# Kernel tuning notes

Hardware: AMD Instinct MI355X
Metric: run time of the kernel (lower is better)

The kernel has to match this reference:

```python
import jax, jax.numpy as jnp
import numpy as np

N_CLUSTERS = 1024
EMBED_DIM = 256
BETA = 0.25
EPS = 1e-05


def setup_inputs() -> dict:
    key = jax.random.key(0)
    k1, k2 = jax.random.split(key)
    z = jax.random.normal(k1, (16, 64, 64, EMBED_DIM), dtype=jnp.float32)
    # nn.init.uniform_(codebook, -1/K, 1/K)
    bound = 1.0 / N_CLUSTERS
    codebook = jax.random.uniform(k2, (N_CLUSTERS, EMBED_DIM), dtype=jnp.float32,
                                  minval=-bound, maxval=bound)
    return {"z": z, "codebook": codebook}


def reference(z, codebook):
    K = codebook.shape[0]
    # squared distances: ||z||^2 + ||e||^2 - 2 z.e  -> [B,V,P,K]
    z2 = jnp.sum(z * z, axis=-1, keepdims=True)          # [B,V,P,1]
    e2 = jnp.sum(codebook * codebook, axis=-1)           # [K]
    ze = jnp.einsum('bvpd,kd->bvpk', z, codebook)        # [B,V,P,K]
    dist = z2 + e2[None, None, None, :] - 2.0 * ze
    indices = jnp.argmin(dist, axis=-1)                  # [B,V,P] int
    z_q = codebook[indices]                              # gather [B,V,P,D]
    z_q_st = z + jax.lax.stop_gradient(z_q - z)          # straight-through

    codebook_loss = jnp.mean((z_q - jax.lax.stop_gradient(z)) ** 2)
    commitment_loss = jnp.mean((z - jax.lax.stop_gradient(z_q)) ** 2)
    cluster_loss = codebook_loss + BETA * commitment_loss

    # perplexity stats (no grad)
    counts = jnp.zeros((K,), dtype=jnp.float32).at[indices.ravel()].add(1.0)
    probs = counts / (counts.sum() + EPS)
    perplexity = jnp.exp(-jnp.sum(probs * jnp.log(probs + EPS)))

    return z_q_st, commitment_loss, codebook_loss, cluster_loss, perplexity, indices
```

## Files before the change

kernel.cpp:

```cpp
#include <hip/hip_runtime.h>
#include <cfloat>
#include <math.h>

#define P_TOT 65536
#define DIM   256
#define KTOT  1024
#define BETA_ 0.25f
#define EPS_  1e-5f
#define MARGIN_ 1.5e-4f

#define OUT_LOSS_OFF ((size_t)P_TOT * DIM)
#define OUT_IDX_OFF  (OUT_LOSS_OFF + 4)

typedef __attribute__((ext_vector_type(8))) short s16x8;
typedef __attribute__((ext_vector_type(4))) float f32x4;

__device__ __forceinline__ unsigned short f2bf(float x) {
    unsigned u = __float_as_uint(x);
    u += 0x7FFFu + ((u >> 16) & 1u);
    return (unsigned short)(u >> 16);
}
__device__ __forceinline__ float bf2f(unsigned short h) {
    return __uint_as_float(((unsigned)h) << 16);
}
__device__ __forceinline__ void gl16(const void* g, void* l) {
    __builtin_amdgcn_global_load_lds(
        (const __attribute__((address_space(1))) unsigned int*)g,
        (__attribute__((address_space(3))) unsigned int*)l, 16, 0, 0);
}

__global__ __launch_bounds__(64) void vq_prep(const float* __restrict__ cb,
                                              float* __restrict__ e2,
                                              unsigned short* __restrict__ cbh,
                                              unsigned short* __restrict__ cbl,
                                              unsigned int* __restrict__ hist,
                                              float* __restrict__ loss_sum,
                                              unsigned int* __restrict__ flag_cnt) {
    const int k = blockIdx.x;
    const int lane = threadIdx.x;
    float4 v = *(const float4*)(cb + (size_t)k * DIM + lane * 4);
    float s = v.x * v.x + v.y * v.y + v.z * v.z + v.w * v.w;
    #pragma unroll
    for (int off = 32; off > 0; off >>= 1) s += __shfl_down(s, off, 64);
    if (lane == 0) e2[k] = s;

    unsigned short h0 = f2bf(v.x), h1 = f2bf(v.y), h2 = f2bf(v.z), h3 = f2bf(v.w);
    unsigned short l0 = f2bf(v.x - bf2f(h0)), l1 = f2bf(v.y - bf2f(h1));
    unsigned short l2 = f2bf(v.z - bf2f(h2)), l3 = f2bf(v.w - bf2f(h3));
    uint2 hp, lp;
    hp.x = (unsigned)h0 | ((unsigned)h1 << 16); hp.y = (unsigned)h2 | ((unsigned)h3 << 16);
    lp.x = (unsigned)l0 | ((unsigned)l1 << 16); lp.y = (unsigned)l2 | ((unsigned)l3 << 16);
    *(uint2*)(cbh + (size_t)k * DIM + lane * 4) = hp;
    *(uint2*)(cbl + (size_t)k * DIM + lane * 4) = lp;

    const int gid = k * 64 + lane;
    if (gid < KTOT) hist[gid] = 0u;
    if (gid == KTOT) { *loss_sum = 0.0f; *flag_cnt = 0u; }
}

__global__ __launch_bounds__(256) void vq_zsplit(const float* __restrict__ z,
                                                 float* __restrict__ z2,
                                                 float* __restrict__ out) {
    const int lane = threadIdx.x & 63;
    const int wave = threadIdx.x >> 6;
    const int p = blockIdx.x * 4 + wave;
    float4 v = *(const float4*)(z + (size_t)p * DIM + lane * 4);
    float s = v.x * v.x + v.y * v.y + v.z * v.z + v.w * v.w;
    #pragma unroll
    for (int off = 32; off > 0; off >>= 1) s += __shfl_down(s, off, 64);
    if (lane == 0) z2[p] = s;

    unsigned short h0 = f2bf(v.x), h1 = f2bf(v.y), h2 = f2bf(v.z), h3 = f2bf(v.w);
    unsigned short l0 = f2bf(v.x - bf2f(h0)), l1 = f2bf(v.y - bf2f(h1));
    unsigned short l2 = f2bf(v.z - bf2f(h2)), l3 = f2bf(v.w - bf2f(h3));
    uint2 hp, lp;
    hp.x = (unsigned)h0 | ((unsigned)h1 << 16); hp.y = (unsigned)h2 | ((unsigned)h3 << 16);
    lp.x = (unsigned)l0 | ((unsigned)l1 << 16); lp.y = (unsigned)l2 | ((unsigned)l3 << 16);
    char* rowb = (char*)out + (size_t)p * 1024;
    *(uint2*)(rowb + lane * 8) = hp;
    *(uint2*)(rowb + 512 + lane * 8) = lp;
}

#define BM 128
#define BN 128

__global__ __launch_bounds__(256, 2) void vq_argmin(
    const float* __restrict__ z, const float* __restrict__ cb,
    const unsigned short* __restrict__ cbh, const unsigned short* __restrict__ cbl,
    const float* __restrict__ z2, const float* __restrict__ e2,
    unsigned int* __restrict__ hist, float* __restrict__ loss_sum,
    unsigned int* __restrict__ flag_cnt, unsigned int* __restrict__ flag_list,
    float* __restrict__ out)
{
    __shared__ __align__(16) char sm[65536];
    __shared__ int kwin[BM];
    __shared__ unsigned char flgs[BM];
    __shared__ float wred[4];

    const int tid = threadIdx.x;
    const int lane = tid & 63;
    const int wid = tid >> 6;
    const int wm = wid >> 1, wn = wid & 1;
    const int col = lane & 15;
    const int lg  = lane >> 4;
    const int swz = lane & 7;
    const int row0 = blockIdx.x * BM;

    const char* zsB  = (const char*)out;
    const char* cbhB = (const char*)cbh;
    const char* cblB = (const char*)cbl;

    float b1[16], b2[16]; int i1[16];
    float z2r[16];
    #pragma unroll
    for (int q = 0; q < 16; ++q) {
        b1[q] = FLT_MAX; b2[q] = FLT_MAX; i1[q] = 0;
        z2r[q] = z2[row0 + wm * 64 + (q >> 2) * 16 + lg * 4 + (q & 3)];
    }

    int aRow[4], bRow[4];
    #pragma unroll
    for (int f = 0; f < 4; ++f) {
        aRow[f] = (wm * 64 + f * 16 + col) * 128;
        bRow[f] = (wn * 64 + f * 16 + col) * 128;
    }
    const int bc0 = ((0 + lg) ^ swz) << 4;
    const int bc1 = ((4 + lg) ^ swz) << 4;

    const int sr  = lane >> 3;
    const int scb = lane & 7;

    #pragma unroll 1
    for (int nc = 0; nc < KTOT / BN; ++nc) {
        const int n0 = nc * BN;
        f32x4 acc[4][4];
        #pragma unroll
        for (int fm = 0; fm < 4; ++fm)
            #pragma unroll
            for (int fn = 0; fn < 4; ++fn)
                acc[fm][fn] = (f32x4){0.0f, 0.0f, 0.0f, 0.0f};

        #pragma unroll 1
        for (int kc = 0; kc < 4; ++kc) {
            __syncthreads();
            #pragma unroll
            for (int i = 0; i < 4; ++i) {
                const int rloc = wid * 32 + i * 8 + sr;
                const int cb16 = ((scb ^ (rloc & 7)) << 4);
                const size_t aoff = ((size_t)(row0 + rloc) << 10) + (kc << 7);
                const size_t boff = ((size_t)(n0 + rloc) << 9) + (kc << 7);
                char* lb = sm + (wid * 32 + i * 8) * 128;
                gl16(zsB + aoff + cb16,        lb);
                gl16(zsB + aoff + 512 + cb16,  lb + 16384);
                gl16(cbhB + boff + cb16,       lb + 32768);
                gl16(cblB + boff + cb16,       lb + 49152);
            }
            __syncthreads();
            #pragma unroll
            for (int ks = 0; ks < 2; ++ks) {
                const int bc = ks ? bc1 : bc0;
                s16x8 ah[4], al[4], bh[4], bl[4];
                #pragma unroll
                for (int f = 0; f < 4; ++f) {
                    ah[f] = *(const s16x8*)(sm + aRow[f] + bc);
                    al[f] = *(const s16x8*)(sm + 16384 + aRow[f] + bc);
                    bh[f] = *(const s16x8*)(sm + 32768 + bRow[f] + bc);
                    bl[f] = *(const s16x8*)(sm + 49152 + bRow[f] + bc);
                }
                #pragma unroll
                for (int fm = 0; fm < 4; ++fm)
                    #pragma unroll
                    for (int fn = 0; fn < 4; ++fn) {
                        acc[fm][fn] = __builtin_amdgcn_mfma_f32_16x16x32_bf16(
                            ah[fm], bh[fn], acc[fm][fn], 0, 0, 0);
                        acc[fm][fn] = __builtin_amdgcn_mfma_f32_16x16x32_bf16(
                            ah[fm], bl[fn], acc[fm][fn], 0, 0, 0);
                        acc[fm][fn] = __builtin_amdgcn_mfma_f32_16x16x32_bf16(
                            al[fm], bh[fn], acc[fm][fn], 0, 0, 0);
                    }
            }
        }
        float e2v[4];
        #pragma unroll
        for (int fn = 0; fn < 4; ++fn) e2v[fn] = e2[n0 + wn * 64 + fn * 16 + col];
        #pragma unroll
        for (int fm = 0; fm < 4; ++fm)
            #pragma unroll
            for (int fn = 0; fn < 4; ++fn)
                #pragma unroll
                for (int r4 = 0; r4 < 4; ++r4) {
                    const int q = fm * 4 + r4;
                    const float dist = (z2r[q] + e2v[fn]) - 2.0f * acc[fm][fn][r4];
                    const int idx = n0 + wn * 64 + fn * 16 + col;
                    if (dist < b1[q]) { b2[q] = b1[q]; b1[q] = dist; i1[q] = idx; }
                    else if (dist < b2[q]) { b2[q] = dist; }
                }
    }

    __syncthreads();
    float* Rb1 = (float*)sm;
    float* Rb2 = (float*)(sm + 16896);
    int*   Ri1 = (int*)(sm + 33792);
    const int slot = col + 16 * wn;
    #pragma unroll
    for (int q = 0; q < 16; ++q) {
        const int px = wm * 64 + (q >> 2) * 16 + lg * 4 + (q & 3);
        Rb1[px * 33 + slot] = b1[q];
        Rb2[px * 33 + slot] = b2[q];
        Ri1[px * 33 + slot] = i1[q];
    }
    __syncthreads();
    if (tid < BM) {
        float x1 = Rb1[tid * 33], x2 = Rb2[tid * 33]; int xi = Ri1[tid * 33];
        for (int s = 1; s < 32; ++s) {
            const float c1 = Rb1[tid * 33 + s], c2 = Rb2[tid * 33 + s];
            const int ci = Ri1[tid * 33 + s];
            const float nb2 = fminf(fmaxf(x1, c1), fminf(x2, c2));
            if (c1 < x1 || (c1 == x1 && ci < xi)) { x1 = c1; xi = ci; }
            x2 = nb2;
        }
        kwin[tid] = xi;
        const bool fl = (x2 - x1) <= MARGIN_;
        flgs[tid] = fl ? 1 : 0;
        if (fl) {
            const unsigned pos = atomicAdd(flag_cnt, 1u);
            flag_list[pos] = (unsigned)(row0 + tid);
        } else {
            out[OUT_IDX_OFF + row0 + tid] = (float)xi;
            atomicAdd(&hist[xi], 1u);
        }
    }
    __syncthreads();

    float lacc = 0.0f;
    #pragma unroll 4
    for (int i = 0; i < 32; ++i) {
        const int flat4 = tid + i * 256;
        const int row = flat4 >> 6;
        if (!flgs[row]) {
            const int dj = (flat4 & 63) * 4;
            const size_t zoff = (size_t)(row0 + row) * DIM + dj;
            float4 zv = *(const float4*)(z + zoff);
            float4 ev = *(const float4*)(cb + (size_t)kwin[row] * DIM + dj);
            float dx = ev.x - zv.x, dy = ev.y - zv.y, dz = ev.z - zv.z, dw = ev.w - zv.w;
            float4 o;
            o.x = zv.x + dx; o.y = zv.y + dy; o.z = zv.z + dz; o.w = zv.w + dw;
            *(float4*)(out + zoff) = o;
            lacc += dx * dx + dy * dy + dz * dz + dw * dw;
        }
    }
    #pragma unroll
    for (int off = 32; off > 0; off >>= 1) lacc += __shfl_down(lacc, off, 64);
    if (lane == 0) wred[wid] = lacc;
    __syncthreads();
    if (tid == 0) atomicAdd(loss_sum, wred[0] + wred[1] + wred[2] + wred[3]);
}

__global__ __launch_bounds__(256) void vq_fix(
    const float* __restrict__ z, const float* __restrict__ cb,
    const float* __restrict__ z2, const float* __restrict__ e2,
    const unsigned int* __restrict__ flag_cnt, const unsigned int* __restrict__ flag_list,
    unsigned int* __restrict__ hist, float* __restrict__ loss_sum,
    float* __restrict__ out)
{
    __shared__ float zrow[4][DIM];
    __shared__ float zz2[4];
    __shared__ int pxid[4];
    __shared__ float rb[4][256];
    __shared__ int   ri[4][256];
    __shared__ int   kw4[4];

    const int tid = threadIdx.x;
    const int total = (int)*flag_cnt;

    for (int base = blockIdx.x * 4; base < total; base += gridDim.x * 4) {
        const int npx = min(4, total - base);
        __syncthreads();
        if (tid < 4) {
            const int p = (int)flag_list[base + (tid < npx ? tid : 0)];
            pxid[tid] = p; zz2[tid] = z2[p];
        }
        __syncthreads();
        {
            const int q = tid >> 6, d = (tid & 63) * 4;
            float4 v = *(const float4*)(z + (size_t)pxid[q] * DIM + d);
            *(float4*)&zrow[q][d] = v;
        }
        __syncthreads();

        const int k0 = tid * 4;
        float acc[4][4];
        #pragma unroll
        for (int q = 0; q < 4; ++q)
            #pragma unroll
            for (int j = 0; j < 4; ++j) acc[q][j] = 0.0f;

        for (int d4 = 0; d4 < 64; ++d4) {
            float4 cv[4];
            #pragma unroll
            for (int j = 0; j < 4; ++j)
                cv[j] = *(const float4*)(cb + (size_t)(k0 + j) * DIM + d4 * 4);
            #pragma unroll
            for (int q = 0; q < 4; ++q) {
                float4 zv = *(const float4*)&zrow[q][d4 * 4];
                #pragma unroll
                for (int j = 0; j < 4; ++j) {
                    acc[q][j] = fmaf(zv.x, cv[j].x, acc[q][j]);
                    acc[q][j] = fmaf(zv.y, cv[j].y, acc[q][j]);
                    acc[q][j] = fmaf(zv.z, cv[j].z, acc[q][j]);
                    acc[q][j] = fmaf(zv.w, cv[j].w, acc[q][j]);
                }
            }
        }
        #pragma unroll
        for (int q = 0; q < 4; ++q) {
            float bd = FLT_MAX; int bi = 0;
            #pragma unroll
            for (int j = 0; j < 4; ++j) {
                const int k = k0 + j;
                const float dist = (zz2[q] + e2[k]) - 2.0f * acc[q][j];
                if (dist < bd) { bd = dist; bi = k; }
            }
            rb[q][tid] = bd; ri[q][tid] = bi;
        }
        __syncthreads();
        {
            const int q = tid >> 6, lane = tid & 63;
            float bd = rb[q][lane]; int bi = ri[q][lane];
            #pragma unroll
            for (int s = 1; s < 4; ++s) {
                const float d2 = rb[q][lane + s * 64]; const int i2 = ri[q][lane + s * 64];
                if (d2 < bd || (d2 == bd && i2 < bi)) { bd = d2; bi = i2; }
            }
            #pragma unroll
            for (int off = 32; off > 0; off >>= 1) {
                const float d2 = __shfl_down(bd, off, 64);
                const int i2 = __shfl_down(bi, off, 64);
                if (d2 < bd || (d2 == bd && i2 < bi)) { bd = d2; bi = i2; }
            }
            if (lane == 0) kw4[q] = bi;
        }
        __syncthreads();
        {
            const int q = tid >> 6, lane = tid & 63;
            if (q < npx) {
                const int p = pxid[q];
                const int kw = kw4[q];
                const int d = lane * 4;
                float4 zv = *(const float4*)&zrow[q][d];
                float4 ev = *(const float4*)(cb + (size_t)kw * DIM + d);
                float dx = ev.x - zv.x, dy = ev.y - zv.y, dz = ev.z - zv.z, dw = ev.w - zv.w;
                float4 o;
                o.x = zv.x + dx; o.y = zv.y + dy; o.z = zv.z + dz; o.w = zv.w + dw;
                *(float4*)(out + (size_t)p * DIM + d) = o;
                float lacc = dx * dx + dy * dy + dz * dz + dw * dw;
                #pragma unroll
                for (int off = 32; off > 0; off >>= 1) lacc += __shfl_down(lacc, off, 64);
                if (lane == 0) {
                    atomicAdd(loss_sum, lacc);
                    out[OUT_IDX_OFF + p] = (float)kw;
                    atomicAdd(&hist[kw], 1u);
                }
            }
        }
    }
}

__global__ __launch_bounds__(1024) void vq_finalize(
    const unsigned int* __restrict__ hist, const float* __restrict__ loss_sum,
    float* __restrict__ out)
{
    __shared__ float sred[16];
    __shared__ float totalsh;
    const int tid = threadIdx.x;
    const float c = (float)hist[tid];

    float t = c;
    #pragma unroll
    for (int off = 32; off > 0; off >>= 1) t += __shfl_down(t, off, 64);
    if ((tid & 63) == 0) sred[tid >> 6] = t;
    __syncthreads();
    if (tid == 0) {
        float s = 0.0f;
        for (int i = 0; i < 16; ++i) s += sred[i];
        totalsh = s;
    }
    __syncthreads();
    const float total = totalsh;
    const float prob = c / (total + EPS_);
    float term = prob * logf(prob + EPS_);
    __syncthreads();
    #pragma unroll
    for (int off = 32; off > 0; off >>= 1) term += __shfl_down(term, off, 64);
    if ((tid & 63) == 0) sred[tid >> 6] = term;
    __syncthreads();
    if (tid == 0) {
        float s = 0.0f;
        for (int i = 0; i < 16; ++i) s += sred[i];
        const float perp = expf(-s);
        const float S = *loss_sum;
        const float mean = S / (float)(P_TOT * DIM);
        out[OUT_LOSS_OFF + 0] = mean;
        out[OUT_LOSS_OFF + 1] = mean;
        out[OUT_LOSS_OFF + 2] = mean + BETA_ * mean;
        out[OUT_LOSS_OFF + 3] = perp;
    }
}

extern "C" void kernel_launch(void* const* d_in, const int* in_sizes, int n_in,
                              void* d_out, int out_size, void* d_ws, size_t ws_size,
                              hipStream_t stream) {
    const float* z  = (const float*)d_in[0];
    const float* cb = (const float*)d_in[1];
    float* out = (float*)d_out;

    float* z2 = (float*)d_ws;
    float* e2 = z2 + P_TOT;
    unsigned int* hist = (unsigned int*)(e2 + KTOT);
    float* loss_sum = (float*)(hist + KTOT);
    unsigned int* flag_cnt = (unsigned int*)(loss_sum + 1);
    unsigned int* flag_list = flag_cnt + 1;
    unsigned short* cbh = (unsigned short*)(((uintptr_t)(flag_list + P_TOT) + 15) & ~(uintptr_t)15);
    unsigned short* cbl = cbh + (size_t)KTOT * DIM;

    vq_prep<<<KTOT, 64, 0, stream>>>(cb, e2, cbh, cbl, hist, loss_sum, flag_cnt);
    vq_zsplit<<<P_TOT / 4, 256, 0, stream>>>(z, z2, out);
    vq_argmin<<<P_TOT / BM, 256, 0, stream>>>(z, cb, cbh, cbl, z2, e2,
                                              hist, loss_sum, flag_cnt, flag_list, out);
    vq_fix<<<1024, 256, 0, stream>>>(z, cb, z2, e2, flag_cnt, flag_list,
                                     hist, loss_sum, out);
    vq_finalize<<<1, 1024, 0, stream>>>(hist, loss_sum, out);
}
```

Measured before the change: 381.8 us.

## Double-buffer LDS staging in argmin GEMM and merge prep kernels

```diff
diff --git a/kernel.cpp b/kernel.cpp
--- a/kernel.cpp
+++ b/kernel.cpp
@@ -29,56 +29,57 @@
         (__attribute__((address_space(3))) unsigned int*)l, 16, 0, 0);
 }
 
-__global__ __launch_bounds__(64) void vq_prep(const float* __restrict__ cb,
-                                              float* __restrict__ e2,
-                                              unsigned short* __restrict__ cbh,
-                                              unsigned short* __restrict__ cbl,
-                                              unsigned int* __restrict__ hist,
-                                              float* __restrict__ loss_sum,
-                                              unsigned int* __restrict__ flag_cnt) {
-    const int k = blockIdx.x;
-    const int lane = threadIdx.x;
-    float4 v = *(const float4*)(cb + (size_t)k * DIM + lane * 4);
-    float s = v.x * v.x + v.y * v.y + v.z * v.z + v.w * v.w;
-    #pragma unroll
-    for (int off = 32; off > 0; off >>= 1) s += __shfl_down(s, off, 64);
-    if (lane == 0) e2[k] = s;
-
-    unsigned short h0 = f2bf(v.x), h1 = f2bf(v.y), h2 = f2bf(v.z), h3 = f2bf(v.w);
-    unsigned short l0 = f2bf(v.x - bf2f(h0)), l1 = f2bf(v.y - bf2f(h1));
-    unsigned short l2 = f2bf(v.z - bf2f(h2)), l3 = f2bf(v.w - bf2f(h3));
-    uint2 hp, lp;
-    hp.x = (unsigned)h0 | ((unsigned)h1 << 16); hp.y = (unsigned)h2 | ((unsigned)h3 << 16);
-    lp.x = (unsigned)l0 | ((unsigned)l1 << 16); lp.y = (unsigned)l2 | ((unsigned)l3 << 16);
-    *(uint2*)(cbh + (size_t)k * DIM + lane * 4) = hp;
-    *(uint2*)(cbl + (size_t)k * DIM + lane * 4) = lp;
-
-    const int gid = k * 64 + lane;
-    if (gid < KTOT) hist[gid] = 0u;
-    if (gid == KTOT) { *loss_sum = 0.0f; *flag_cnt = 0u; }
-}
-
-__global__ __launch_bounds__(256) void vq_zsplit(const float* __restrict__ z,
-                                                 float* __restrict__ z2,
-                                                 float* __restrict__ out) {
-    const int lane = threadIdx.x & 63;
-    const int wave = threadIdx.x >> 6;
-    const int p = blockIdx.x * 4 + wave;
-    float4 v = *(const float4*)(z + (size_t)p * DIM + lane * 4);
-    float s = v.x * v.x + v.y * v.y + v.z * v.z + v.w * v.w;
-    #pragma unroll
-    for (int off = 32; off > 0; off >>= 1) s += __shfl_down(s, off, 64);
-    if (lane == 0) z2[p] = s;
-
-    unsigned short h0 = f2bf(v.x), h1 = f2bf(v.y), h2 = f2bf(v.z), h3 = f2bf(v.w);
-    unsigned short l0 = f2bf(v.x - bf2f(h0)), l1 = f2bf(v.y - bf2f(h1));
-    unsigned short l2 = f2bf(v.z - bf2f(h2)), l3 = f2bf(v.w - bf2f(h3));
-    uint2 hp, lp;
-    hp.x = (unsigned)h0 | ((unsigned)h1 << 16); hp.y = (unsigned)h2 | ((unsigned)h3 << 16);
-    lp.x = (unsigned)l0 | ((unsigned)l1 << 16); lp.y = (unsigned)l2 | ((unsigned)l3 << 16);
-    char* rowb = (char*)out + (size_t)p * 1024;
-    *(uint2*)(rowb + lane * 8) = hp;
-    *(uint2*)(rowb + 512 + lane * 8) = lp;
+__global__ __launch_bounds__(256) void vq_pre(
+    const float* __restrict__ z, const float* __restrict__ cb,
+    float* __restrict__ z2, float* __restrict__ e2,
+    char* __restrict__ cbi, unsigned int* __restrict__ hist,
+    float* __restrict__ loss_sum, unsigned int* __restrict__ flag_cnt,
+    float* __restrict__ out)
+{
+    const int tid = threadIdx.x;
+    const int lane = tid & 63;
+    const int wave = tid >> 6;
+    const int bid = blockIdx.x;
+
+    if (bid < P_TOT / 4) {
+        const int p = bid * 4 + wave;
+        float4 v = *(const float4*)(z + (size_t)p * DIM + lane * 4);
+        float s = v.x * v.x + v.y * v.y + v.z * v.z + v.w * v.w;
+        #pragma unroll
+        for (int off = 32; off > 0; off >>= 1) s += __shfl_down(s, off, 64);
+        if (lane == 0) z2[p] = s;
+
+        unsigned short h0 = f2bf(v.x), h1 = f2bf(v.y), h2 = f2bf(v.z), h3 = f2bf(v.w);
+        unsigned short l0 = f2bf(v.x - bf2f(h0)), l1 = f2bf(v.y - bf2f(h1));
+        unsigned short l2 = f2bf(v.z - bf2f(h2)), l3 = f2bf(v.w - bf2f(h3));
+        uint2 hp, lp;
+        hp.x = (unsigned)h0 | ((unsigned)h1 << 16); hp.y = (unsigned)h2 | ((unsigned)h3 << 16);
+        lp.x = (unsigned)l0 | ((unsigned)l1 << 16); lp.y = (unsigned)l2 | ((unsigned)l3 << 16);
+        char* rowb = (char*)out + (size_t)p * 1024;
+        *(uint2*)(rowb + lane * 8) = hp;
+        *(uint2*)(rowb + 512 + lane * 8) = lp;
+    } else {
+        const int rel = bid - P_TOT / 4;
+        const int k = rel * 4 + wave;
+        float4 v = *(const float4*)(cb + (size_t)k * DIM + lane * 4);
+        float s = v.x * v.x + v.y * v.y + v.z * v.z + v.w * v.w;
+        #pragma unroll
+        for (int off = 32; off > 0; off >>= 1) s += __shfl_down(s, off, 64);
+        if (lane == 0) e2[k] = s;
+
+        unsigned short h0 = f2bf(v.x), h1 = f2bf(v.y), h2 = f2bf(v.z), h3 = f2bf(v.w);
+        unsigned short l0 = f2bf(v.x - bf2f(h0)), l1 = f2bf(v.y - bf2f(h1));
+        unsigned short l2 = f2bf(v.z - bf2f(h2)), l3 = f2bf(v.w - bf2f(h3));
+        uint2 hp, lp;
+        hp.x = (unsigned)h0 | ((unsigned)h1 << 16); hp.y = (unsigned)h2 | ((unsigned)h3 << 16);
+        lp.x = (unsigned)l0 | ((unsigned)l1 << 16); lp.y = (unsigned)l2 | ((unsigned)l3 << 16);
+        char* rowb = cbi + (size_t)k * 1024;
+        *(uint2*)(rowb + lane * 8) = hp;
+        *(uint2*)(rowb + 512 + lane * 8) = lp;
+
+        if (rel < 4) hist[rel * 256 + tid] = 0u;
+        if (rel == 4 && tid == 0) { *loss_sum = 0.0f; *flag_cnt = 0u; }
+    }
 }
 
 #define BM 128
@@ -86,7 +87,7 @@
 
 __global__ __launch_bounds__(256, 2) void vq_argmin(
     const float* __restrict__ z, const float* __restrict__ cb,
-    const unsigned short* __restrict__ cbh, const unsigned short* __restrict__ cbl,
+    const char* __restrict__ cbi,
     const float* __restrict__ z2, const float* __restrict__ e2,
     unsigned int* __restrict__ hist, float* __restrict__ loss_sum,
     unsigned int* __restrict__ flag_cnt, unsigned int* __restrict__ flag_list,
@@ -103,12 +104,9 @@
     const int wm = wid >> 1, wn = wid & 1;
     const int col = lane & 15;
     const int lg  = lane >> 4;
-    const int swz = lane & 7;
     const int row0 = blockIdx.x * BM;
 
-    const char* zsB  = (const char*)out;
-    const char* cbhB = (const char*)cbh;
-    const char* cblB = (const char*)cbl;
+    const char* zsB = (const char*)out;
 
     float b1[16], b2[16]; int i1[16];
     float z2r[16];
@@ -118,83 +116,97 @@
         z2r[q] = z2[row0 + wm * 64 + (q >> 2) * 16 + lg * 4 + (q & 3)];
     }
 
-    int aRow[4], bRow[4];
+    int aOff[4], bOff[4];
     #pragma unroll
     for (int f = 0; f < 4; ++f) {
-        aRow[f] = (wm * 64 + f * 16 + col) * 128;
-        bRow[f] = (wn * 64 + f * 16 + col) * 128;
-    }
-    const int bc0 = ((0 + lg) ^ swz) << 4;
-    const int bc1 = ((4 + lg) ^ swz) << 4;
-
-    const int sr  = lane >> 3;
-    const int scb = lane & 7;
-
-    #pragma unroll 1
-    for (int nc = 0; nc < KTOT / BN; ++nc) {
-        const int n0 = nc * BN;
-        f32x4 acc[4][4];
+        const int pbl = (lg ^ (col & 7)) << 4;
+        aOff[f] = (wm * 64 + f * 16 + col) * 128 + pbl;
+        bOff[f] = (wn * 64 + f * 16 + col) * 128 + pbl;
+    }
+
+    const int sr = lane >> 3;
+    const int pb = lane & 7;
+    const int lb = pb ^ sr;
+    const int srcColBase = ((lb & 4) << 7) + ((lb & 3) << 4);
+
+    auto STAGE = [&](int buf, int step) {
+        const int nc = step >> 3, k8 = step & 7;
+        const int srcCol = k8 * 64 + srcColBase;
+        char* ab = sm + (buf << 15);
+        const size_t brow0 = (size_t)(nc << 7) << 10;
+        #pragma unroll
+        for (int i = 0; i < 4; ++i) {
+            const int r = i * 32 + wid * 8 + sr;
+            char* ldst = ab + (i * 32 + wid * 8) * 128;
+            gl16(zsB + (((size_t)(row0 + r)) << 10) + srcCol, ldst);
+            gl16(cbi + brow0 + (((size_t)r) << 10) + srcCol, ldst + 16384);
+        }
+    };
+
+    f32x4 acc[4][4];
+
+    STAGE(0, 0);
+    __syncthreads();
+
+    #pragma unroll 2
+    for (int t = 0; t < 64; ++t) {
+        const int b = t & 1;
+        if ((t & 7) == 0) {
+            #pragma unroll
+            for (int fm = 0; fm < 4; ++fm)
+                #pragma unroll
+                for (int fn = 0; fn < 4; ++fn)
+                    acc[fm][fn] = (f32x4){0.0f, 0.0f, 0.0f, 0.0f};
+        }
+        float ef0 = 0.f, ef1 = 0.f, ef2 = 0.f, ef3 = 0.f;
+        if ((t & 7) == 7) {
+            const float* ep = e2 + ((t >> 3) << 7) + wn * 64 + col;
+            ef0 = ep[0]; ef1 = ep[16]; ef2 = ep[32]; ef3 = ep[48];
+        }
+        if (t < 63) STAGE(b ^ 1, t + 1);
+        __builtin_amdgcn_sched_barrier(0);
+
+        const char* ab = sm + (b << 15);
+        s16x8 ah[4], al[4], bh[4], bl[4];
+        #pragma unroll
+        for (int f = 0; f < 4; ++f) {
+            ah[f] = *(const s16x8*)(ab + aOff[f]);
+            al[f] = *(const s16x8*)(ab + (aOff[f] ^ 64));
+            bh[f] = *(const s16x8*)(ab + 16384 + bOff[f]);
+            bl[f] = *(const s16x8*)(ab + 16384 + (bOff[f] ^ 64));
+        }
         #pragma unroll
         for (int fm = 0; fm < 4; ++fm)
             #pragma unroll
-            for (int fn = 0; fn < 4; ++fn)
-                acc[fm][fn] = (f32x4){0.0f, 0.0f, 0.0f, 0.0f};
-
-        #pragma unroll 1
-        for (int kc = 0; kc < 4; ++kc) {
-            __syncthreads();
-            #pragma unroll
-            for (int i = 0; i < 4; ++i) {
-                const int rloc = wid * 32 + i * 8 + sr;
-                const int cb16 = ((scb ^ (rloc & 7)) << 4);
-                const size_t aoff = ((size_t)(row0 + rloc) << 10) + (kc << 7);
-                const size_t boff = ((size_t)(n0 + rloc) << 9) + (kc << 7);
-                char* lb = sm + (wid * 32 + i * 8) * 128;
-                gl16(zsB + aoff + cb16,        lb);
-                gl16(zsB + aoff + 512 + cb16,  lb + 16384);
-                gl16(cbhB + boff + cb16,       lb + 32768);
-                gl16(cblB + boff + cb16,       lb + 49152);
-            }
-            __syncthreads();
-            #pragma unroll
-            for (int ks = 0; ks < 2; ++ks) {
-                const int bc = ks ? bc1 : bc0;
-                s16x8 ah[4], al[4], bh[4], bl[4];
+            for (int fn = 0; fn < 4; ++fn) {
+                acc[fm][fn] = __builtin_amdgcn_mfma_f32_16x16x32_bf16(
+                    ah[fm], bh[fn], acc[fm][fn], 0, 0, 0);
+                acc[fm][fn] = __builtin_amdgcn_mfma_f32_16x16x32_bf16(
+                    ah[fm], bl[fn], acc[fm][fn], 0, 0, 0);
+                acc[fm][fn] = __builtin_amdgcn_mfma_f32_16x16x32_bf16(
+                    al[fm], bh[fn], acc[fm][fn], 0, 0, 0);
+            }
+
+        if ((t & 7) == 7) {
+            const int n0 = (t >> 3) << 7;
+            const float ef[4] = {ef0, ef1, ef2, ef3};
+            #pragma unroll
+            for (int fm = 0; fm < 4; ++fm)
                 #pragma unroll
-                for (int f = 0; f < 4; ++f) {
-                    ah[f] = *(const s16x8*)(sm + aRow[f] + bc);
-                    al[f] = *(const s16x8*)(sm + 16384 + aRow[f] + bc);
-                    bh[f] = *(const s16x8*)(sm + 32768 + bRow[f] + bc);
-                    bl[f] = *(const s16x8*)(sm + 49152 + bRow[f] + bc);
-                }
-                #pragma unroll
-                for (int fm = 0; fm < 4; ++fm)
+                for (int fn = 0; fn < 4; ++fn)
                     #pragma unroll
-                    for (int fn = 0; fn < 4; ++fn) {
-                        acc[fm][fn] = __builtin_amdgcn_mfma_f32_16x16x32_bf16(
-                            ah[fm], bh[fn], acc[fm][fn], 0, 0, 0);
-                        acc[fm][fn] = __builtin_amdgcn_mfma_f32_16x16x32_bf16(
-                            ah[fm], bl[fn], acc[fm][fn], 0, 0, 0);
-                        acc[fm][fn] = __builtin_amdgcn_mfma_f32_16x16x32_bf16(
-                            al[fm], bh[fn], acc[fm][fn], 0, 0, 0);
+                    for (int r4 = 0; r4 < 4; ++r4) {
+                        const int q = fm * 4 + r4;
+                        const float dist = (z2r[q] + ef[fn]) - 2.0f * acc[fm][fn][r4];
+                        const int idx = n0 + wn * 64 + fn * 16 + col;
+                        if (dist < b1[q]) { b2[q] = b1[q]; b1[q] = dist; i1[q] = idx; }
+                        else if (dist < b2[q]) { b2[q] = dist; }
                     }
-            }
-        }
-        float e2v[4];
-        #pragma unroll
-        for (int fn = 0; fn < 4; ++fn) e2v[fn] = e2[n0 + wn * 64 + fn * 16 + col];
-        #pragma unroll
-        for (int fm = 0; fm < 4; ++fm)
-            #pragma unroll
-            for (int fn = 0; fn < 4; ++fn)
-                #pragma unroll
-                for (int r4 = 0; r4 < 4; ++r4) {
-                    const int q = fm * 4 + r4;
-                    const float dist = (z2r[q] + e2v[fn]) - 2.0f * acc[fm][fn][r4];
-                    const int idx = n0 + wn * 64 + fn * 16 + col;
-                    if (dist < b1[q]) { b2[q] = b1[q]; b1[q] = dist; i1[q] = idx; }
-                    else if (dist < b2[q]) { b2[q] = dist; }
-                }
+        }
+        __builtin_amdgcn_sched_barrier(0);
+        asm volatile("s_waitcnt vmcnt(0)" ::: "memory");
+        __builtin_amdgcn_s_barrier();
+        __builtin_amdgcn_sched_barrier(0);
     }
 
     __syncthreads();
@@ -420,12 +432,11 @@
     float* loss_sum = (float*)(hist + KTOT);
     unsigned int* flag_cnt = (unsigned int*)(loss_sum + 1);
     unsigned int* flag_list = flag_cnt + 1;
-    unsigned short* cbh = (unsigned short*)(((uintptr_t)(flag_list + P_TOT) + 15) & ~(uintptr_t)15);
-    unsigned short* cbl = cbh + (size_t)KTOT * DIM;
-
-    vq_prep<<<KTOT, 64, 0, stream>>>(cb, e2, cbh, cbl, hist, loss_sum, flag_cnt);
-    vq_zsplit<<<P_TOT / 4, 256, 0, stream>>>(z, z2, out);
-    vq_argmin<<<P_TOT / BM, 256, 0, stream>>>(z, cb, cbh, cbl, z2, e2,
+    char* cbi = (char*)(((uintptr_t)(flag_list + P_TOT) + 15) & ~(uintptr_t)15);
+
+    vq_pre<<<P_TOT / 4 + KTOT / 4, 256, 0, stream>>>(z, cb, z2, e2, cbi, hist,
+                                                     loss_sum, flag_cnt, out);
+    vq_argmin<<<P_TOT / BM, 256, 0, stream>>>(z, cb, cbi, z2, e2,
                                               hist, loss_sum, flag_cnt, flag_list, out);
     vq_fix<<<1024, 256, 0, stream>>>(z, cb, z2, e2, flag_cnt, flag_list,
                                      hist, loss_sum, out);
```

Measured after the change: 430.6 us. +12.8%, slower.
